# Kernel tuning notes

Measured on AMD Instinct MI355X. Metric: run time of the kernel, lower is better.

The kernel has to match this reference:

```python
import jax, jax.numpy as jnp
import numpy as np

N_QUBITS = 14
W_MUL = (2.0 ** 0.5) * (5.0 ** -0.5)  # he_std = gain * 5**-0.5, lrmul = 1
TWO_PI = 2.0 * np.pi


def _rx(t):
    c = jnp.cos(t / 2); s = jnp.sin(t / 2)
    return jnp.stack([jnp.stack([c + 0j, -1j * s]), jnp.stack([-1j * s, c + 0j])])


def _ry(t):
    c = jnp.cos(t / 2); s = jnp.sin(t / 2)
    return jnp.stack([jnp.stack([c + 0j, -s + 0j]), jnp.stack([s + 0j, c + 0j])])


def _rz(t):
    e = jnp.exp(-0.5j * t); z = jnp.zeros_like(e)
    return jnp.stack([jnp.stack([e, z]), jnp.stack([z, jnp.conj(e)])])


def _apply_1q(state, gate, q):
    # state: (B,) + (2,)*n ; apply 2x2 gate on qubit q (axis q+1)
    ax = q + 1
    out = jnp.tensordot(gate, state, axes=([1], [ax]))  # new qubit axis at front
    return jnp.moveaxis(out, 0, ax)


_CNOT = jnp.array([[1, 0, 0, 0],
                   [0, 1, 0, 0],
                   [0, 0, 0, 1],
                   [0, 0, 1, 0]], dtype=jnp.complex64).reshape(2, 2, 2, 2)


def _apply_cnot(state, c, t):
    # _CNOT indices: [out_c, out_t, in_c, in_t]
    out = jnp.tensordot(_CNOT, state, axes=([2, 3], [c + 1, t + 1]))
    return jnp.moveaxis(out, (0, 1), (c + 1, t + 1))


def _rot_layer(state, params, gates):
    # per-qubit triple of rotations: params[3*i + j] for gate j on qubit i
    for i in range(N_QUBITS):
        for j, g in enumerate(gates):
            state = _apply_1q(state, g(params[3 * i + j]), i)
    return state


def _ring_of_cnot(state):
    for i in range(N_QUBITS):
        state = _apply_cnot(state, i, (i + 1) % N_QUBITS)
    return state


def _forward(x_real, x_imag, weight):
    n = N_QUBITS
    B = x_real.shape[0]
    psi = (x_real + 1j * x_imag).astype(jnp.complex64).reshape((B,) + (2,) * n)
    w = weight * W_MUL
    layers = [(_rx, _ry, _rz),  # XYZLayer
              (_ry, _rz, _ry),  # YZYLayer
              (_rz, _ry, _rx),  # ZYXLayer
              (_rx, _rz, _rx),  # XZXLayer
              (_ry, _rz, _ry)]  # YZYLayer
    for li, gates in enumerate(layers):
        psi = _rot_layer(psi, w[3 * n * li: 3 * n * (li + 1)], gates)
        if li < len(layers) - 1:
            psi = _ring_of_cnot(psi)
    Z = jnp.array([[1, 0], [0, -1]], dtype=jnp.complex64)
    zpsi = _apply_1q(psi, Z, 0)
    # <psi| Z_0 |psi> (original: conj(psi) row-vector @ (Z_0 psi) column-vector, take real)
    ev = jnp.sum(jnp.conj(psi) * zpsi, axis=tuple(range(1, n + 1))).real
    return ev.reshape(B, 1)  # matches torch (B,1,1).squeeze(-1)


def setup_inputs() -> dict:
    key = jax.random.key(0)
    k1, k2, k3 = jax.random.split(key, 3)
    B = 512
    dim = 2 ** N_QUBITS
    x_real = jax.random.normal(k1, (B, 1, dim), dtype=jnp.float32)
    x_imag = jax.random.normal(k2, (B, 1, dim), dtype=jnp.float32)
    weight = jax.random.uniform(k3, (15 * N_QUBITS,), dtype=jnp.float32) * TWO_PI
    return {"x_real": x_real, "x_imag": x_imag, "weight": weight}


def reference(x_real, x_imag, weight):
    return _forward(x_real, x_imag, weight)
```

## Files before the change

kernel.cpp:

```cpp
#include <hip/hip_runtime.h>
#include <hip/hip_bf16.h>

#define NQ   14
#define DIM  16384
#define BLK  1024
#define WMUL 0.6324555320336759f

typedef float v2f __attribute__((ext_vector_type(2)));

struct C2 { float x, y; };
__device__ inline C2 cmulc(C2 a, C2 b){ return C2{a.x*b.x - a.y*b.y, a.x*b.y + a.y*b.x}; }
__device__ inline C2 caddc(C2 a, C2 b){ return C2{a.x+b.x, a.y+b.y}; }
__device__ inline void mm2(const C2* a, const C2* b, C2* o) {
    o[0] = caddc(cmulc(a[0],b[0]), cmulc(a[1],b[2]));
    o[1] = caddc(cmulc(a[0],b[1]), cmulc(a[1],b[3]));
    o[2] = caddc(cmulc(a[2],b[0]), cmulc(a[3],b[2]));
    o[3] = caddc(cmulc(a[2],b[1]), cmulc(a[3],b[3]));
}
__device__ inline void build_gate(int ty, float t, C2* g) {
    float sn, cs;
    __sincosf(0.5f * t, &sn, &cs);
    if (ty == 0) {
        g[0] = C2{cs, 0.f}; g[1] = C2{0.f, -sn};
        g[2] = C2{0.f, -sn}; g[3] = C2{cs, 0.f};
    } else if (ty == 1) {
        g[0] = C2{cs, 0.f}; g[1] = C2{-sn, 0.f};
        g[2] = C2{sn, 0.f}; g[3] = C2{cs, 0.f};
    } else {
        g[0] = C2{cs, -sn}; g[1] = C2{0.f, 0.f};
        g[2] = C2{0.f, 0.f}; g[3] = C2{cs, sn};
    }
}
__device__ const int TYPES[5][3] = {
    {0,1,2},
    {1,2,1},
    {2,1,0},
    {0,2,0},
    {1,2,1},
};

__device__ inline constexpr uint32_t slotf(uint32_t i){
    return i ^ (((i>>4) ^ (i>>8) ^ (i>>12)) & 15u);
}
template<int B> __device__ inline uint32_t ins0(uint32_t t){
    return ((t & ~((1u<<B)-1u)) << 1) | (t & ((1u<<B)-1u));
}
template<int B0,int B1,int B2> __device__ inline uint32_t expand3(uint32_t t){
    return ins0<B2>(ins0<B1>(ins0<B0>(t)));
}
template<int B0,int B1,int B2> __device__ inline constexpr uint32_t rmask3(int r){
    return ((r&1)?(1u<<B0):0u) | ((r&2)?(1u<<B1):0u) | ((r&4)?(1u<<B2):0u);
}

template<int J>
__device__ inline void rot8(v2f* v, const v2f* __restrict__ g){
    const v2f a00=g[0], b00=g[1], a01=g[2], b01=g[3];
    const v2f a10=g[4], b10=g[5], a11=g[6], b11=g[7];
    #pragma unroll
    for (int r = 0; r < 8; ++r){
        if (!(r & (1 << J))) {
            v2f x0 = v[r], x1 = v[r | (1 << J)];
            v2f s0 = x0.yx, s1 = x1.yx;
            v2f y0 = a00*x0 + b00*s0 + a01*x1 + b01*s1;
            v2f y1 = a10*x0 + b10*s0 + a11*x1 + b11*s1;
            v[r] = y0; v[r | (1<<J)] = y1;
        }
    }
}
template<int C, int T>
__device__ inline void cnot8(v2f* v){
    #pragma unroll
    for (int r = 0; r < 8; ++r){
        if ((r & (1 << C)) && !(r & (1 << T))) {
            v2f tt = v[r]; v[r] = v[r | (1 << T)]; v[r | (1 << T)] = tt;
        }
    }
}

__global__ __launch_bounds__(BLK) void qsim_kernel(
        const float* __restrict__ xr, const float* __restrict__ xi,
        const float* __restrict__ w, float* __restrict__ out) {
    __shared__ v2f s[DIM];
    __shared__ v2f gmp[5 * NQ * 8];
    __shared__ float meas[4];
    __shared__ float red[BLK / 64];

    const int b   = blockIdx.x;
    const uint32_t tid = threadIdx.x;

    if (tid < 5 * NQ) {
        const int li = tid / NQ, q = tid % NQ;
        C2 M[4], G[4], T[4];
        #pragma unroll
        for (int j = 0; j < 3; ++j) {
            float t = w[3 * NQ * li + 3 * q + j] * WMUL;
            build_gate(TYPES[li][j], t, G);
            if (j == 0) { M[0]=G[0]; M[1]=G[1]; M[2]=G[2]; M[3]=G[3]; }
            else { mm2(G, M, T); M[0]=T[0]; M[1]=T[1]; M[2]=T[2]; M[3]=T[3]; }
        }
        #pragma unroll
        for (int k = 0; k < 4; ++k) {
            gmp[tid * 8 + k * 2 + 0] = v2f{ M[k].x, M[k].x};
            gmp[tid * 8 + k * 2 + 1] = v2f{-M[k].y, M[k].y};
        }
        if (tid == 4 * NQ + 0) {
            meas[0] = M[0].x*M[0].x + M[0].y*M[0].y - (M[2].x*M[2].x + M[2].y*M[2].y);
            meas[1] = M[1].x*M[1].x + M[1].y*M[1].y - (M[3].x*M[3].x + M[3].y*M[3].y);
            meas[2] = (M[0].x*M[1].x + M[0].y*M[1].y) - (M[2].x*M[3].x + M[2].y*M[3].y);
            meas[3] = (M[0].x*M[1].y - M[0].y*M[1].x) - (M[2].x*M[3].y - M[2].y*M[3].x);
        }
    }
    __syncthreads();

    const float* xrb = xr + (size_t)b * DIM;
    const float* xib = xi + (size_t)b * DIM;

    #define GMP(li, q) (&gmp[((li) * NQ + (q)) * 8])

    #define PASS(B0, B1, B2, ...)                                                  \
        _Pragma("unroll 1")                                                        \
        for (uint32_t sl = 0; sl < 2; ++sl) {                                      \
            const uint32_t t  = tid + sl * BLK;                                    \
            const uint32_t sb = slotf(expand3<B0,B1,B2>(t));                       \
            v2f v[8];                                                              \
            _Pragma("unroll")                                                      \
            for (int r = 0; r < 8; ++r)                                            \
                v[r] = s[sb ^ slotf(rmask3<B0,B1,B2>(r))];                         \
            __VA_ARGS__                                                            \
            _Pragma("unroll")                                                      \
            for (int r = 0; r < 8; ++r)                                            \
                s[sb ^ slotf(rmask3<B0,B1,B2>(r))] = v[r];                         \
        }                                                                          \
        __syncthreads();

    float local = 0.f;

    #pragma unroll 1
    for (int li = 0; li < 4; ++li) {
        #pragma unroll 1
        for (uint32_t sl = 0; sl < 2; ++sl) {
            const uint32_t t = tid + sl * BLK;
            v2f v[8];
            if (li == 0) {
                #pragma unroll
                for (int r = 0; r < 8; ++r) {
                    uint32_t i = t | ((uint32_t)r << 11);
                    v[r] = v2f{xrb[i], xib[i]};
                }
            } else {
                const uint32_t sb = slotf(expand3<11,12,13>(t));
                #pragma unroll
                for (int r = 0; r < 8; ++r)
                    v[r] = s[sb ^ slotf(rmask3<11,12,13>(r))];
            }
            rot8<2>(v, GMP(li,0)); rot8<1>(v, GMP(li,1)); rot8<0>(v, GMP(li,2));
            cnot8<2,1>(v); cnot8<1,0>(v);
            const uint32_t sb = slotf(expand3<11,12,13>(t));
            #pragma unroll
            for (int r = 0; r < 8; ++r)
                s[sb ^ slotf(rmask3<11,12,13>(r))] = v[r];
        }
        __syncthreads();

        PASS(9,10,11, rot8<1>(v, GMP(li,3));  rot8<0>(v, GMP(li,4));  cnot8<2,1>(v); cnot8<1,0>(v);)
        PASS(7,8,9,   rot8<1>(v, GMP(li,5));  rot8<0>(v, GMP(li,6));  cnot8<2,1>(v); cnot8<1,0>(v);)
        PASS(5,6,7,   rot8<1>(v, GMP(li,7));  rot8<0>(v, GMP(li,8));  cnot8<2,1>(v); cnot8<1,0>(v);)
        PASS(3,4,5,   rot8<1>(v, GMP(li,9));  rot8<0>(v, GMP(li,10)); cnot8<2,1>(v); cnot8<1,0>(v);)
        PASS(1,2,3,   rot8<1>(v, GMP(li,11)); rot8<0>(v, GMP(li,12)); cnot8<2,1>(v); cnot8<1,0>(v);)

        #pragma unroll 1
        for (uint32_t sl = 0; sl < 2; ++sl) {
            const uint32_t t  = tid + sl * BLK;
            const uint32_t sb = slotf(expand3<0,1,13>(t));
            v2f v[8];
            #pragma unroll
            for (int r = 0; r < 8; ++r)
                v[r] = s[sb ^ slotf(rmask3<0,1,13>(r))];
            rot8<0>(v, GMP(li,13));
            cnot8<1,0>(v); cnot8<0,2>(v);
            if (li < 3) {
                #pragma unroll
                for (int r = 0; r < 8; ++r)
                    s[sb ^ slotf(rmask3<0,1,13>(r))] = v[r];
            } else {
                const float mA = meas[0], mB = meas[1], mP = meas[2], mQ = meas[3];
                #pragma unroll
                for (int r = 0; r < 4; ++r) {
                    v2f a0 = v[r], a1 = v[r | 4];
                    float n0 = a0.x*a0.x + a0.y*a0.y;
                    float n1 = a1.x*a1.x + a1.y*a1.y;
                    float u  = a0.x*a1.x + a0.y*a1.y;
                    float vv = a0.x*a1.y - a0.y*a1.x;
                    local += mA*n0 + mB*n1 + 2.f*(mP*u - mQ*vv);
                }
            }
        }
        if (li < 3) __syncthreads();
    }

    #pragma unroll
    for (int off = 32; off > 0; off >>= 1) local += __shfl_down(local, off);
    const int lane = tid & 63, wid = tid >> 6;
    if (lane == 0) red[wid] = local;
    __syncthreads();
    if (tid == 0) {
        float t = 0.f;
        #pragma unroll
        for (int k = 0; k < BLK / 64; ++k) t += red[k];
        out[b] = t;
    }
}

extern "C" void kernel_launch(void* const* d_in, const int* in_sizes, int n_in,
                              void* d_out, int out_size, void* d_ws, size_t ws_size,
                              hipStream_t stream) {
    const float* xr = (const float*)d_in[0];
    const float* xi = (const float*)d_in[1];
    const float* w  = (const float*)d_in[2];
    float* out = (float*)d_out;
    const int B = out_size;
    qsim_kernel<<<B, BLK, 0, stream>>>(xr, xi, w, out);
}
```

Baseline: 115.2 us.

## Merge gate passes to three qubits each using thread-indexed controlled swaps

Regroups the per-layer shared-memory passes so each middle pass applies rotations on three qubits instead of two. The CNOT whose control lies outside the register tile becomes a thread-index-selected swap. This cuts the number of shared-memory load/store sweeps and block barriers per layer. In exchange it adds select instructions and more register work per pass.

```diff
diff --git a/kernel.cpp b/kernel.cpp
--- a/kernel.cpp
+++ b/kernel.cpp
@@ -73,6 +73,17 @@
     for (int r = 0; r < 8; ++r){
         if ((r & (1 << C)) && !(r & (1 << T))) {
             v2f tt = v[r]; v[r] = v[r | (1 << T)]; v[r | (1 << T)] = tt;
+        }
+    }
+}
+template<int T>
+__device__ inline void cnotSel(v2f* v, bool c){
+    #pragma unroll
+    for (int r = 0; r < 8; ++r){
+        if (!(r & (1 << T))) {
+            v2f lo = v[r], hi = v[r | (1 << T)];
+            v[r]          = c ? hi : lo;
+            v[r | (1<<T)] = c ? lo : hi;
         }
     }
 }
@@ -162,12 +173,21 @@
         }
         __syncthreads();
 
-        PASS(9,10,11, rot8<1>(v, GMP(li,3));  rot8<0>(v, GMP(li,4));  cnot8<2,1>(v); cnot8<1,0>(v);)
-        PASS(7,8,9,   rot8<1>(v, GMP(li,5));  rot8<0>(v, GMP(li,6));  cnot8<2,1>(v); cnot8<1,0>(v);)
-        PASS(5,6,7,   rot8<1>(v, GMP(li,7));  rot8<0>(v, GMP(li,8));  cnot8<2,1>(v); cnot8<1,0>(v);)
-        PASS(3,4,5,   rot8<1>(v, GMP(li,9));  rot8<0>(v, GMP(li,10)); cnot8<2,1>(v); cnot8<1,0>(v);)
-        PASS(1,2,3,   rot8<1>(v, GMP(li,11)); rot8<0>(v, GMP(li,12)); cnot8<2,1>(v); cnot8<1,0>(v);)
-
+        PASS(8,9,10,
+            rot8<2>(v, GMP(li,3)); rot8<1>(v, GMP(li,4)); rot8<0>(v, GMP(li,5));
+            cnotSel<2>(v, (t >> 8) & 1u);
+            cnot8<2,1>(v); cnot8<1,0>(v);
+        )
+        PASS(5,6,7,
+            rot8<2>(v, GMP(li,6)); rot8<1>(v, GMP(li,7)); rot8<0>(v, GMP(li,8));
+            cnotSel<2>(v, (t >> 5) & 1u);
+            cnot8<2,1>(v); cnot8<1,0>(v);
+        )
+        PASS(2,3,4,
+            rot8<2>(v, GMP(li,9)); rot8<1>(v, GMP(li,10)); rot8<0>(v, GMP(li,11));
+            cnotSel<2>(v, (t >> 2) & 1u);
+            cnot8<2,1>(v); cnot8<1,0>(v);
+        )
         #pragma unroll 1
         for (uint32_t sl = 0; sl < 2; ++sl) {
             const uint32_t t  = tid + sl * BLK;
@@ -176,8 +196,10 @@
             #pragma unroll
             for (int r = 0; r < 8; ++r)
                 v[r] = s[sb ^ slotf(rmask3<0,1,13>(r))];
-            rot8<0>(v, GMP(li,13));
-            cnot8<1,0>(v); cnot8<0,2>(v);
+            rot8<1>(v, GMP(li,12)); rot8<0>(v, GMP(li,13));
+            cnotSel<1>(v, t & 1u);
+            cnot8<1,0>(v);
+            cnot8<0,2>(v);
             if (li < 3) {
                 #pragma unroll
                 for (int r = 0; r < 8; ++r)
```

After: 114.1 us. About the same (-1.0%).
